# Kernel tuning notes

Hardware: AMD Instinct MI355X
Metric: run time of the kernel (lower is better)

The kernel has to match this reference:

```python
import jax, jax.numpy as jnp
import numpy as np

DIM = 1024
HEADS = 16
HEAD_DIM = DIM // HEADS
MLP_HIDDEN = DIM * 4
EPS = 1e-6


def _ln(x):
    # LayerNorm without affine, eps=1e-6
    mu = jnp.mean(x, axis=-1, keepdims=True)
    var = jnp.var(x, axis=-1, keepdims=True)
    return (x - mu) / jnp.sqrt(var + EPS)


def setup_inputs() -> dict:
    key = jax.random.key(0)
    ks = jax.random.split(key, 12)
    B, N = 8, 1024
    s = lambda fan: 1.0 / np.sqrt(fan)
    return {
        "x": jax.random.normal(ks[0], (B, N, DIM), jnp.float32),
        "c": jax.random.normal(ks[1], (B, DIM), jnp.float32),
        "w_qkv": jax.random.normal(ks[2], (DIM, 3 * DIM), jnp.float32) * s(DIM),
        "b_qkv": jnp.zeros((3 * DIM,), jnp.float32),
        "w_proj": jax.random.normal(ks[3], (DIM, DIM), jnp.float32) * s(DIM),
        "b_proj": jnp.zeros((DIM,), jnp.float32),
        "w_mlp1": jax.random.normal(ks[4], (DIM, MLP_HIDDEN), jnp.float32) * s(DIM),
        "b_mlp1": jnp.zeros((MLP_HIDDEN,), jnp.float32),
        "w_mlp2": jax.random.normal(ks[5], (MLP_HIDDEN, DIM), jnp.float32) * s(MLP_HIDDEN),
        "b_mlp2": jnp.zeros((DIM,), jnp.float32),
        "w_ada": jax.random.normal(ks[6], (DIM, 6 * DIM), jnp.float32) * s(DIM),
        "b_ada": jnp.zeros((6 * DIM,), jnp.float32),
    }


def _attention(h, w_qkv, b_qkv, w_proj, b_proj):
    B, N, C = h.shape
    qkv = h @ w_qkv + b_qkv  # [B,N,3C]
    qkv = qkv.reshape(B, N, 3, HEADS, HEAD_DIM)
    q, k, v = qkv[:, :, 0], qkv[:, :, 1], qkv[:, :, 2]  # [B,N,H,Dh]
    scale = HEAD_DIM ** -0.5
    attn = jnp.einsum("bqhd,bkhd->bhqk", q, k) * scale
    attn = jax.nn.softmax(attn, axis=-1)
    o = jnp.einsum("bhqk,bkhd->bqhd", attn, v).reshape(B, N, C)
    return o @ w_proj + b_proj


def reference(x, c, w_qkv, b_qkv, w_proj, b_proj, w_mlp1, b_mlp1, w_mlp2, b_mlp2, w_ada, b_ada):
    mod = (jax.nn.silu(c) @ w_ada + b_ada)[:, None, :]  # [B,1,6D]
    g1, be1, a1, g2, be2, a2 = jnp.split(mod, 6, axis=-1)
    h = _ln(x) * (1.0 + g1) + be1
    x = x + a1 * _attention(h, w_qkv, b_qkv, w_proj, b_proj)
    h = _ln(x) * (1.0 + g2) + be2
    mlp = jax.nn.gelu(h @ w_mlp1 + b_mlp1, approximate=False) @ w_mlp2 + b_mlp2
    return x + a2 * mlp
```

## Files before the change

kernel.cpp:

```cpp
#include <hip/hip_runtime.h>
#include <hip/hip_bf16.h>

#define DIMC 1024
#define SEQ  1024
#define NB   8
#define NH   16
#define HD2  64
#define EPSV 1e-6f

typedef short short8 __attribute__((ext_vector_type(8)));
typedef float floatx4 __attribute__((ext_vector_type(4)));

#define GLOAD_LDS(g, l) \
  __builtin_amdgcn_global_load_lds((const __attribute__((address_space(1))) unsigned int*)(g), \
                                   (__attribute__((address_space(3))) unsigned int*)(l), 16, 0, 0)

__device__ __forceinline__ float bf2f(unsigned short u){
  union { float f; unsigned int i; } v; v.i = ((unsigned int)u) << 16; return v.f;
}
__device__ __forceinline__ unsigned short f2bf(float f){
  union { float f; unsigned int i; } v; v.f = f;
  unsigned int r = v.i + 0x7fffu + ((v.i >> 16) & 1u);
  return (unsigned short)(r >> 16);
}

__global__ __launch_bounds__(256)
void tcvt_kernel(const float* __restrict__ in, unsigned short* __restrict__ out, int K, int N)
{
  __shared__ float tile[32][33];
  const int n0 = blockIdx.x * 32;
  const int k0 = blockIdx.y * 32;
  const int tx = threadIdx.x & 31;
  const int ty = threadIdx.x >> 5;
#pragma unroll
  for (int i = 0; i < 4; i++)
    tile[ty + i*8][tx] = in[(size_t)(k0 + ty + i*8) * N + n0 + tx];
  __syncthreads();
#pragma unroll
  for (int i = 0; i < 4; i++)
    out[(size_t)(n0 + ty + i*8) * K + k0 + tx] = f2bf(tile[tx][ty + i*8]);
}

__global__ __launch_bounds__(256)
void ada1_kernel(const float* __restrict__ c,
                 const float* __restrict__ w_ada,
                 float* __restrict__ partial)
{
  __shared__ float cs[NB][128];
  const int chunk = blockIdx.y;
  const int col = blockIdx.x * 256 + threadIdx.x;
  const int t = threadIdx.x;
  for (int i = t; i < NB * 128; i += 256) {
    const int b = i >> 7, k = i & 127;
    const float v = c[b * DIMC + chunk * 128 + k];
    cs[b][k] = v / (1.0f + __expf(-v));
  }
  __syncthreads();
  float acc[NB];
#pragma unroll
  for (int b = 0; b < NB; b++) acc[b] = 0.0f;
#pragma unroll 8
  for (int k = 0; k < 128; k++) {
    const float wv = w_ada[(size_t)(chunk * 128 + k) * 6144 + col];
#pragma unroll
    for (int b = 0; b < NB; b++) acc[b] = fmaf(cs[b][k], wv, acc[b]);
  }
#pragma unroll
  for (int b = 0; b < NB; b++)
    partial[((size_t)chunk * NB + b) * 6144 + col] = acc[b];
}

__global__ __launch_bounds__(256)
void ada2_kernel(const float* __restrict__ partial, const float* __restrict__ b_ada,
                 float* __restrict__ mod)
{
  const int i = blockIdx.x * 256 + threadIdx.x;
  const int b = i / 6144, col = i % 6144;
  float s = b_ada[col];
#pragma unroll
  for (int ch = 0; ch < 8; ch++) s += partial[((size_t)ch * NB + b) * 6144 + col];
  mod[i] = s;
}

__global__ __launch_bounds__(256)
void ln_kernel(const float* __restrict__ xin, const float* __restrict__ mod,
               int goff, int boff, unsigned short* __restrict__ hout)
{
  const int row = blockIdx.x;
  const int bb = row >> 10;
  const int t = threadIdx.x;
  const float4 x4 = *((const float4*)(xin + (size_t)row * DIMC) + t);
  const float v0 = x4.x, v1 = x4.y, v2 = x4.z, v3 = x4.w;
  float s  = v0 + v1 + v2 + v3;
  float ss = v0*v0 + v1*v1 + v2*v2 + v3*v3;
#pragma unroll
  for (int off = 32; off > 0; off >>= 1) {
    s  += __shfl_down(s,  off, 64);
    ss += __shfl_down(ss, off, 64);
  }
  __shared__ float red[10];
  const int w = t >> 6;
  if ((t & 63) == 0) { red[w] = s; red[4 + w] = ss; }
  __syncthreads();
  if (t == 0) {
    const float S  = red[0] + red[1] + red[2] + red[3];
    const float SS = red[4] + red[5] + red[6] + red[7];
    const float mu = S * (1.0f / 1024.0f);
    red[8] = mu;
    red[9] = rsqrtf(SS * (1.0f / 1024.0f) - mu * mu + EPSV);
  }
  __syncthreads();
  const float mu = red[8], rstd = red[9];
  const float* mrow = mod + (size_t)bb * 6144;
  const int d = t * 4;
  const float h0 = (v0 - mu) * rstd * (1.0f + mrow[goff + d + 0]) + mrow[boff + d + 0];
  const float h1 = (v1 - mu) * rstd * (1.0f + mrow[goff + d + 1]) + mrow[boff + d + 1];
  const float h2 = (v2 - mu) * rstd * (1.0f + mrow[goff + d + 2]) + mrow[boff + d + 2];
  const float h3 = (v3 - mu) * rstd * (1.0f + mrow[goff + d + 3]) + mrow[boff + d + 3];
  uint2 u;
  u.x = (unsigned)f2bf(h0) | ((unsigned)f2bf(h1) << 16);
  u.y = (unsigned)f2bf(h2) | ((unsigned)f2bf(h3) << 16);
  *((uint2*)(hout + (size_t)row * DIMC + d)) = u;
}

template<int MODE>
__global__ __launch_bounds__(256, 2)
void gemm_kernel(const unsigned short* __restrict__ A,
                 const unsigned short* __restrict__ Bt,
                 const float* __restrict__ bias,
                 void* __restrict__ Cout,
                 const float* __restrict__ resid,
                 const float* __restrict__ mod,
                 int M, int N, int K, int SH)
{
  __shared__ unsigned short As[128 * 32];
  __shared__ unsigned short Bs[128 * 32];
  const int tid = threadIdx.x;

  const int nT = N >> 7;
  const int mT = M >> 7;
  const int mb = mT >> 3;
  const int bid = blockIdx.x;
  const int xcd = bid & 7;
  const int slot = bid >> 3;
  const int sgroup = slot / (SH * nT);
  const int rem = slot - sgroup * (SH * nT);
  const int ni = rem / SH;
  const int mi = sgroup * SH + rem - ni * SH;
  const int m0 = (xcd * mb + mi) * 128;
  const int n0 = ni * 128;

  const int wid = tid >> 6;
  const int lane = tid & 63;
  const int quad = lane >> 4;
  const int c16 = lane & 15;
  const int wr = (wid >> 1) * 64;
  const int wc = (wid & 1) * 64;
  const int srow = lane >> 2;
  const int scol = (lane & 3) * 8;
  const unsigned short* aG = A  + (size_t)(m0 + wid * 32 + srow) * K + scol;
  const unsigned short* bG = Bt + (size_t)(n0 + wid * 32 + srow) * K + scol;
  unsigned short* AsW = As + wid * 32 * 32;
  unsigned short* BsW = Bs + wid * 32 * 32;

  floatx4 acc[4][4];
#pragma unroll
  for (int i = 0; i < 4; i++)
#pragma unroll
    for (int j = 0; j < 4; j++) acc[i][j] = (floatx4)(0.0f);

  for (int k0 = 0; k0 < K; k0 += 32) {
    GLOAD_LDS(aG + k0,            AsW);
    GLOAD_LDS(aG + 16 * K + k0,   AsW + 16 * 32);
    GLOAD_LDS(bG + k0,            BsW);
    GLOAD_LDS(bG + 16 * K + k0,   BsW + 16 * 32);
    __syncthreads();

    short8 af[4], bfv[4];
#pragma unroll
    for (int i = 0; i < 4; i++)
      af[i] = *(const short8*)&As[(wr + i * 16 + c16) * 32 + quad * 8];
#pragma unroll
    for (int j = 0; j < 4; j++)
      bfv[j] = *(const short8*)&Bs[(wc + j * 16 + c16) * 32 + quad * 8];
#pragma unroll
    for (int i = 0; i < 4; i++)
#pragma unroll
      for (int j = 0; j < 4; j++)
        acc[i][j] = __builtin_amdgcn_mfma_f32_16x16x32_bf16(af[i], bfv[j], acc[i][j], 0, 0, 0);
    __syncthreads();
  }

  const int bb = m0 >> 10;
#pragma unroll
  for (int j = 0; j < 4; j++) {
    const int col = n0 + wc + j * 16 + c16;
    const float bv = bias[col];
#pragma unroll
    for (int i = 0; i < 4; i++) {
      const int rowb = m0 + wr + i * 16 + quad * 4;
#pragma unroll
      for (int r = 0; r < 4; r++) {
        const int row = rowb + r;
        const size_t idx = (size_t)row * N + col;
        float v = acc[i][j][r] + bv;
        if (MODE == 0) {
          ((unsigned short*)Cout)[idx] = f2bf(v);
        } else if (MODE == 1) {
          v = 0.5f * v * (1.0f + erff(v * 0.70710678f));
          ((unsigned short*)Cout)[idx] = f2bf(v);
        } else if (MODE == 2) {
          const float a = mod[(size_t)bb * 6144 + 2048 + col];
          ((float*)Cout)[idx] = fmaf(a, v, resid[idx]);
        } else {
          const float a = mod[(size_t)bb * 6144 + 5120 + col];
          ((float*)Cout)[idx] = fmaf(a, v, resid[idx]);
        }
      }
    }
  }
}

__global__ __launch_bounds__(256, 2)
void fattn_kernel(const unsigned short* __restrict__ qkv, unsigned short* __restrict__ o_out)
{
  __shared__ unsigned short Ks[64][72];
  __shared__ unsigned short Vt[64][72];
  __shared__ unsigned short Pt[4][32][72];

  const int blk = blockIdx.x;
  const int qt = blk & 7;
  const int h  = (blk >> 3) & 15;
  const int bb = blk >> 7;
  const int tid = threadIdx.x;
  const int w = tid >> 6;
  const int lane = tid & 63;
  const int quad = lane >> 4;
  const int c16 = lane & 15;
  const int q0 = qt * 128 + w * 32;

  short8 qf[2][2];
#pragma unroll
  for (int msub = 0; msub < 2; msub++)
#pragma unroll
    for (int kh = 0; kh < 2; kh++) {
      const size_t idx = ((size_t)((bb*SEQ + q0 + msub*16 + c16) * 3 + 0)) * DIMC
                       + h * HD2 + kh * 32 + quad * 8;
      const uint4 u = *(const uint4*)(qkv + idx);
      const unsigned short* pu = (const unsigned short*)&u;
      short8 r;
#pragma unroll
      for (int j = 0; j < 8; j++) r[j] = (short)f2bf(bf2f(pu[j]) * 0.125f);
      qf[msub][kh] = r;
    }

  floatx4 oacc[2][4];
  float lsum[2][4];
#pragma unroll
  for (int msub = 0; msub < 2; msub++) {
#pragma unroll
    for (int r = 0; r < 4; r++) lsum[msub][r] = 0.0f;
#pragma unroll
    for (int d = 0; d < 4; d++) oacc[msub][d] = (floatx4)(0.0f);
  }

  const int tok = tid & 63;
  const int dg = tid >> 6;

  for (int kt = 0; kt < 16; kt++) {
    __syncthreads();
    {
      const size_t base = ((size_t)((bb*SEQ + kt*64 + tok) * 3)) * DIMC + h * HD2 + dg * 16;
      const uint4 ku0 = *(const uint4*)(qkv + base + DIMC);
      const uint4 ku1 = *(const uint4*)(qkv + base + DIMC + 8);
      const uint4 vu0 = *(const uint4*)(qkv + base + 2*DIMC);
      const uint4 vu1 = *(const uint4*)(qkv + base + 2*DIMC + 8);
      *(uint4*)&Ks[tok][dg*16]     = ku0;
      *(uint4*)&Ks[tok][dg*16 + 8] = ku1;
      const unsigned short* vp0 = (const unsigned short*)&vu0;
      const unsigned short* vp1 = (const unsigned short*)&vu1;
#pragma unroll
      for (int j = 0; j < 8; j++) Vt[dg*16 + j][tok] = vp0[j];
#pragma unroll
      for (int j = 0; j < 8; j++) Vt[dg*16 + 8 + j][tok] = vp1[j];
    }
    __syncthreads();

    floatx4 s[2][4];
#pragma unroll
    for (int msub = 0; msub < 2; msub++)
#pragma unroll
      for (int nsub = 0; nsub < 4; nsub++) s[msub][nsub] = (floatx4)(0.0f);
#pragma unroll
    for (int nsub = 0; nsub < 4; nsub++) {
      const short8 kf0 = *(const short8*)&Ks[nsub*16 + c16][quad*8];
      const short8 kf1 = *(const short8*)&Ks[nsub*16 + c16][32 + quad*8];
#pragma unroll
      for (int msub = 0; msub < 2; msub++) {
        s[msub][nsub] = __builtin_amdgcn_mfma_f32_16x16x32_bf16(qf[msub][0], kf0, s[msub][nsub], 0, 0, 0);
        s[msub][nsub] = __builtin_amdgcn_mfma_f32_16x16x32_bf16(qf[msub][1], kf1, s[msub][nsub], 0, 0, 0);
      }
    }

#pragma unroll
    for (int msub = 0; msub < 2; msub++)
#pragma unroll
      for (int nsub = 0; nsub < 4; nsub++)
#pragma unroll
        for (int r = 0; r < 4; r++) {
          const float p = __expf(s[msub][nsub][r] - 8.0f);
          lsum[msub][r] += p;
          Pt[w][msub*16 + quad*4 + r][nsub*16 + c16] = f2bf(p);
        }

    short8 pa[2][2];
#pragma unroll
    for (int msub = 0; msub < 2; msub++) {
      pa[msub][0] = *(const short8*)&Pt[w][msub*16 + c16][quad*8];
      pa[msub][1] = *(const short8*)&Pt[w][msub*16 + c16][32 + quad*8];
    }
#pragma unroll
    for (int dsub = 0; dsub < 4; dsub++) {
      const short8 vf0 = *(const short8*)&Vt[dsub*16 + c16][quad*8];
      const short8 vf1 = *(const short8*)&Vt[dsub*16 + c16][32 + quad*8];
#pragma unroll
      for (int msub = 0; msub < 2; msub++) {
        oacc[msub][dsub] = __builtin_amdgcn_mfma_f32_16x16x32_bf16(pa[msub][0], vf0, oacc[msub][dsub], 0, 0, 0);
        oacc[msub][dsub] = __builtin_amdgcn_mfma_f32_16x16x32_bf16(pa[msub][1], vf1, oacc[msub][dsub], 0, 0, 0);
      }
    }
  }

#pragma unroll
  for (int msub = 0; msub < 2; msub++) {
    float rl[4];
#pragma unroll
    for (int r = 0; r < 4; r++) {
      float t = lsum[msub][r];
#pragma unroll
      for (int xm = 1; xm < 16; xm <<= 1) t += __shfl_xor(t, xm, 64);
      rl[r] = 1.0f / t;
    }
#pragma unroll
    for (int dsub = 0; dsub < 4; dsub++)
#pragma unroll
      for (int r = 0; r < 4; r++) {
        const size_t idx = (size_t)(bb*SEQ + q0 + msub*16 + quad*4 + r) * DIMC
                         + h * HD2 + dsub*16 + c16;
        o_out[idx] = f2bf(oacc[msub][dsub][r] * rl[r]);
      }
  }
}

extern "C" void kernel_launch(void* const* d_in, const int* in_sizes, int n_in,
                              void* d_out, int out_size, void* d_ws, size_t ws_size,
                              hipStream_t stream) {
  const float* x      = (const float*)d_in[0];
  const float* c      = (const float*)d_in[1];
  const float* w_qkv  = (const float*)d_in[2];
  const float* b_qkv  = (const float*)d_in[3];
  const float* w_proj = (const float*)d_in[4];
  const float* b_proj = (const float*)d_in[5];
  const float* w_mlp1 = (const float*)d_in[6];
  const float* b_mlp1 = (const float*)d_in[7];
  const float* w_mlp2 = (const float*)d_in[8];
  const float* b_mlp2 = (const float*)d_in[9];
  const float* w_ada  = (const float*)d_in[10];
  const float* b_ada  = (const float*)d_in[11];

  char* ws = (char*)d_ws;
  float*          mod     = (float*)(ws);
  unsigned short* wqkv_t  = (unsigned short*)(ws + 196608);
  unsigned short* wproj_t = (unsigned short*)(ws + 6488064);
  unsigned short* wmlp1_t = (unsigned short*)(ws + 8585216);
  unsigned short* wmlp2_t = (unsigned short*)(ws + 16973824);
  unsigned short* bufH    = (unsigned short*)(ws + 25362432);
  float*          adapart = (float*)(ws + 25362432);
  unsigned short* qkv     = (unsigned short*)(ws + 42139648);
  unsigned short* hid     = (unsigned short*)(ws + 42139648);
  float*          out     = (float*)d_out;

  const int M = NB * SEQ;

  tcvt_kernel<<<dim3(96, 32),  256, 0, stream>>>(w_qkv,  wqkv_t,  1024, 3072);
  tcvt_kernel<<<dim3(32, 32),  256, 0, stream>>>(w_proj, wproj_t, 1024, 1024);
  tcvt_kernel<<<dim3(128, 32), 256, 0, stream>>>(w_mlp1, wmlp1_t, 1024, 4096);
  tcvt_kernel<<<dim3(32, 128), 256, 0, stream>>>(w_mlp2, wmlp2_t, 4096, 1024);

  ada1_kernel<<<dim3(24, 8), 256, 0, stream>>>(c, w_ada, adapart);
  ada2_kernel<<<192, 256, 0, stream>>>(adapart, b_ada, mod);

  ln_kernel<<<M, 256, 0, stream>>>(x, mod, 0, 1024, bufH);
  gemm_kernel<0><<<24 * 64, 256, 0, stream>>>(bufH, wqkv_t, b_qkv, qkv, nullptr, nullptr, M, 3072, 1024, 8);
  fattn_kernel<<<1024, 256, 0, stream>>>(qkv, bufH);
  gemm_kernel<2><<<8 * 64, 256, 0, stream>>>(bufH, wproj_t, b_proj, out, x, mod, M, 1024, 1024, 8);
  ln_kernel<<<M, 256, 0, stream>>>(out, mod, 3072, 4096, bufH);

  const size_t fullHidEnd = 42139648ull + (size_t)M * 4096 * 2;
  if (ws_size >= fullHidEnd) {
    gemm_kernel<1><<<32 * 64, 256, 0, stream>>>(bufH, wmlp1_t, b_mlp1, hid,
                                                nullptr, nullptr, M, 4096, 1024, 8);
    gemm_kernel<3><<<8 * 64, 256, 0, stream>>>(hid, wmlp2_t, b_mlp2, out,
                                               out, mod, M, 1024, 4096, 2);
  } else {
    for (int half = 0; half < 2; half++) {
      const size_t roff = (size_t)half * 4096;
      gemm_kernel<1><<<32 * 32, 256, 0, stream>>>(bufH + roff * DIMC, wmlp1_t, b_mlp1, hid,
                                                  nullptr, nullptr, 4096, 4096, 1024, 4);
      gemm_kernel<3><<<8 * 32, 256, 0, stream>>>(hid, wmlp2_t, b_mlp2, out + roff * DIMC,
                                                 out + roff * DIMC, mod + (size_t)half * 4 * 6144,
                                                 4096, 1024, 4096, 2);
    }
  }
}
```

Before: 556.0 us.

## Replace 128x128 GEMM with double-buffered 256x256 tile, 8-wave pipelined kernel

Rewrites the GEMM as a 256x256 output tile with 512 threads and a K-step of 64. LDS is double-buffered and XOR-swizzled, and the global->LDS loads for the next k-slice are interleaved with MFMA phases under explicit barriers, vmcnt waits and setprio. Larger tiles raise operand reuse per byte loaded, and the software pipelining hides load latency behind MFMA work. In exchange it uses 128KB of LDS per block and heavy register pressure. Grid sizes shrink, for example only 128 blocks for the N=1024 GEMMs, which may leave CUs idle.

```diff
diff --git a/kernel.cpp b/kernel.cpp
--- a/kernel.cpp
+++ b/kernel.cpp
@@ -123,82 +123,134 @@
   *((uint2*)(hout + (size_t)row * DIMC + d)) = u;
 }
 
+#define MF(a, b, c) __builtin_amdgcn_mfma_f32_16x16x32_bf16(a, b, c, 0, 0, 0)
+#define FENCE() asm volatile("" ::: "memory")
+#define BARRIER() do { FENCE(); __builtin_amdgcn_s_barrier(); FENCE(); } while (0)
+
 template<int MODE>
-__global__ __launch_bounds__(256, 2)
-void gemm_kernel(const unsigned short* __restrict__ A,
-                 const unsigned short* __restrict__ Bt,
-                 const float* __restrict__ bias,
-                 void* __restrict__ Cout,
-                 const float* __restrict__ resid,
-                 const float* __restrict__ mod,
-                 int M, int N, int K, int SH)
-{
-  __shared__ unsigned short As[128 * 32];
-  __shared__ unsigned short Bs[128 * 32];
-  const int tid = threadIdx.x;
-
-  const int nT = N >> 7;
-  const int mT = M >> 7;
+__global__ __launch_bounds__(512, 2)
+void gemm256_kernel(const unsigned short* __restrict__ A,
+                    const unsigned short* __restrict__ Bt,
+                    const float* __restrict__ bias,
+                    void* __restrict__ Cout,
+                    const float* __restrict__ resid,
+                    const float* __restrict__ mod,
+                    int M, int N, int K)
+{
+  __shared__ unsigned short As[2][16384];
+  __shared__ unsigned short Bs[2][16384];
+
+  const int mT = M >> 8;
   const int mb = mT >> 3;
   const int bid = blockIdx.x;
   const int xcd = bid & 7;
-  const int slot = bid >> 3;
-  const int sgroup = slot / (SH * nT);
-  const int rem = slot - sgroup * (SH * nT);
-  const int ni = rem / SH;
-  const int mi = sgroup * SH + rem - ni * SH;
-  const int m0 = (xcd * mb + mi) * 128;
-  const int n0 = ni * 128;
-
-  const int wid = tid >> 6;
-  const int lane = tid & 63;
-  const int quad = lane >> 4;
-  const int c16 = lane & 15;
-  const int wr = (wid >> 1) * 64;
-  const int wc = (wid & 1) * 64;
-  const int srow = lane >> 2;
-  const int scol = (lane & 3) * 8;
-  const unsigned short* aG = A  + (size_t)(m0 + wid * 32 + srow) * K + scol;
-  const unsigned short* bG = Bt + (size_t)(n0 + wid * 32 + srow) * K + scol;
-  unsigned short* AsW = As + wid * 32 * 32;
-  unsigned short* BsW = Bs + wid * 32 * 32;
-
-  floatx4 acc[4][4];
-#pragma unroll
-  for (int i = 0; i < 4; i++)
+  const int local = bid >> 3;
+  const int ni = local / mb;
+  const int mi = xcd * mb + (local - ni * mb);
+  const int m0 = mi << 8, n0 = ni << 8;
+
+  const int tid = threadIdx.x;
+  const int w = tid >> 6, lane = tid & 63;
+  const int quad = lane >> 4, c16 = lane & 15;
+  const int wm = w >> 2, wn = w & 3, w2 = w << 1;
+
+  const int aRow = wm * 8192 + c16 * 64;
+  const int bRow = (wn >> 1) * 8192 + ((wn & 1) * 64 + c16) * 64;
+  const int sxz  = (c16 & 7) << 4;
+  const int swz0 = ((0  + quad * 16) ^ sxz) >> 1;
+  const int swz1 = ((64 + quad * 16) ^ sxz) >> 1;
+#define LDA8(cc, i, SW) (*(const short8*)&As[cc][aRow + (i) * 1024 + (SW)])
+#define LDB8(cc, j, SW) (*(const short8*)&Bs[cc][bRow + (j) * 1024 + (SW)])
+
+  const int l8 = lane >> 3, lc = lane & 7;
+  const int stC = ((lc ^ l8) << 3);
+  const unsigned short* aSt = A  + (size_t)(m0 + w2 * 8 + l8) * K + stC;
+  const unsigned short* bSt = Bt + (size_t)(n0 + w2 * 8 + l8) * K + stC;
+#define STAGE_A(cc, h, kk0) do { \
+  GLOAD_LDS(aSt + (size_t)((h) * 128    ) * K + (kk0), &As[cc][(h) * 8192 + w2 * 512      ]); \
+  GLOAD_LDS(aSt + (size_t)((h) * 128 + 8) * K + (kk0), &As[cc][(h) * 8192 + w2 * 512 + 512]); \
+} while (0)
+#define STAGE_B(cc, h, kk0) do { \
+  GLOAD_LDS(bSt + (size_t)((h) * 128    ) * K + (kk0), &Bs[cc][(h) * 8192 + w2 * 512      ]); \
+  GLOAD_LDS(bSt + (size_t)((h) * 128 + 8) * K + (kk0), &Bs[cc][(h) * 8192 + w2 * 512 + 512]); \
+} while (0)
+
+  floatx4 acc[8][4];
+#pragma unroll
+  for (int i = 0; i < 8; i++)
 #pragma unroll
     for (int j = 0; j < 4; j++) acc[i][j] = (floatx4)(0.0f);
 
-  for (int k0 = 0; k0 < K; k0 += 32) {
-    GLOAD_LDS(aG + k0,            AsW);
-    GLOAD_LDS(aG + 16 * K + k0,   AsW + 16 * 32);
-    GLOAD_LDS(bG + k0,            BsW);
-    GLOAD_LDS(bG + 16 * K + k0,   BsW + 16 * 32);
-    __syncthreads();
-
-    short8 af[4], bfv[4];
-#pragma unroll
-    for (int i = 0; i < 4; i++)
-      af[i] = *(const short8*)&As[(wr + i * 16 + c16) * 32 + quad * 8];
-#pragma unroll
-    for (int j = 0; j < 4; j++)
-      bfv[j] = *(const short8*)&Bs[(wc + j * 16 + c16) * 32 + quad * 8];
-#pragma unroll
-    for (int i = 0; i < 4; i++)
-#pragma unroll
-      for (int j = 0; j < 4; j++)
-        acc[i][j] = __builtin_amdgcn_mfma_f32_16x16x32_bf16(af[i], bfv[j], acc[i][j], 0, 0, 0);
-    __syncthreads();
+#define MMROW(i, aE, aO) do { \
+  acc[i][0] = MF(aE, bF00, acc[i][0]); acc[i][0] = MF(aO, bF01, acc[i][0]); \
+  acc[i][1] = MF(aE, bF10, acc[i][1]); acc[i][1] = MF(aO, bF11, acc[i][1]); \
+  acc[i][2] = MF(aE, bF20, acc[i][2]); acc[i][2] = MF(aO, bF21, acc[i][2]); \
+  acc[i][3] = MF(aE, bF30, acc[i][3]); acc[i][3] = MF(aO, bF31, acc[i][3]); \
+} while (0)
+
+#define PH_TAIL(i0, i1) do { \
+  BARRIER(); \
+  asm volatile("s_waitcnt lgkmcnt(0)" ::: "memory"); \
+  __builtin_amdgcn_s_setprio(1); \
+  MMROW(i0, a0, a1); \
+  MMROW(i1, a2, a3); \
+  __builtin_amdgcn_s_setprio(0); \
+} while (0)
+
+#define GROUP(cc, oo, g) do { \
+  const int kA_ = ((g) + 1) << 6; const int kB_ = ((g) + 2) << 6; \
+  const bool dA_ = kA_ < K; const bool dB_ = kB_ < K; \
+  short8 bF00 = LDB8(cc, 0, swz0), bF01 = LDB8(cc, 0, swz1); \
+  short8 bF10 = LDB8(cc, 1, swz0), bF11 = LDB8(cc, 1, swz1); \
+  short8 bF20 = LDB8(cc, 2, swz0), bF21 = LDB8(cc, 2, swz1); \
+  short8 bF30 = LDB8(cc, 3, swz0), bF31 = LDB8(cc, 3, swz1); \
+  short8 a0 = LDA8(cc, 0, swz0), a1 = LDA8(cc, 0, swz1); \
+  short8 a2 = LDA8(cc, 1, swz0), a3 = LDA8(cc, 1, swz1); \
+  if (dA_) STAGE_A(oo, 0, kA_); \
+  PH_TAIL(0, 1); \
+  BARRIER(); \
+  a0 = LDA8(cc, 2, swz0); a1 = LDA8(cc, 2, swz1); \
+  a2 = LDA8(cc, 3, swz0); a3 = LDA8(cc, 3, swz1); \
+  if (dA_) STAGE_A(oo, 1, kA_); \
+  PH_TAIL(2, 3); \
+  BARRIER(); \
+  a0 = LDA8(cc, 4, swz0); a1 = LDA8(cc, 4, swz1); \
+  a2 = LDA8(cc, 5, swz0); a3 = LDA8(cc, 5, swz1); \
+  if (dB_) STAGE_B(cc, 0, kB_); \
+  PH_TAIL(4, 5); \
+  BARRIER(); \
+  a0 = LDA8(cc, 6, swz0); a1 = LDA8(cc, 6, swz1); \
+  a2 = LDA8(cc, 7, swz0); a3 = LDA8(cc, 7, swz1); \
+  if (dB_) STAGE_B(cc, 1, kB_); \
+  PH_TAIL(6, 7); \
+  if (dB_) { asm volatile("s_waitcnt vmcnt(4)" ::: "memory"); } \
+  else     { asm volatile("s_waitcnt vmcnt(0)" ::: "memory"); } \
+  BARRIER(); \
+} while (0)
+
+  STAGE_B(0, 0, 0);  STAGE_B(0, 1, 0);
+  STAGE_A(0, 0, 0);  STAGE_A(0, 1, 0);
+  STAGE_B(1, 0, 64); STAGE_B(1, 1, 64);
+  asm volatile("s_waitcnt vmcnt(4)" ::: "memory");
+  BARRIER();
+
+  const int T = K >> 6;
+  for (int g = 0; g < T; g += 2) {
+    GROUP(0, 1, g);
+    GROUP(1, 0, g + 1);
   }
 
   const int bb = m0 >> 10;
 #pragma unroll
   for (int j = 0; j < 4; j++) {
-    const int col = n0 + wc + j * 16 + c16;
+    const int col = n0 + wn * 64 + j * 16 + c16;
     const float bv = bias[col];
-#pragma unroll
-    for (int i = 0; i < 4; i++) {
-      const int rowb = m0 + wr + i * 16 + quad * 4;
+    float av = 0.0f;
+    if (MODE == 2) av = mod[(size_t)bb * 6144 + 2048 + col];
+    if (MODE == 3) av = mod[(size_t)bb * 6144 + 5120 + col];
+#pragma unroll
+    for (int i = 0; i < 8; i++) {
+      const int rowb = m0 + wm * 128 + i * 16 + quad * 4;
 #pragma unroll
       for (int r = 0; r < 4; r++) {
         const int row = rowb + r;
@@ -209,16 +261,19 @@
         } else if (MODE == 1) {
           v = 0.5f * v * (1.0f + erff(v * 0.70710678f));
           ((unsigned short*)Cout)[idx] = f2bf(v);
-        } else if (MODE == 2) {
-          const float a = mod[(size_t)bb * 6144 + 2048 + col];
-          ((float*)Cout)[idx] = fmaf(a, v, resid[idx]);
         } else {
-          const float a = mod[(size_t)bb * 6144 + 5120 + col];
-          ((float*)Cout)[idx] = fmaf(a, v, resid[idx]);
+          ((float*)Cout)[idx] = fmaf(av, v, resid[idx]);
         }
       }
     }
   }
+#undef GROUP
+#undef PH_TAIL
+#undef MMROW
+#undef STAGE_A
+#undef STAGE_B
+#undef LDA8
+#undef LDB8
 }
 
 __global__ __launch_bounds__(256, 2)
@@ -391,25 +446,25 @@
   ada2_kernel<<<192, 256, 0, stream>>>(adapart, b_ada, mod);
 
   ln_kernel<<<M, 256, 0, stream>>>(x, mod, 0, 1024, bufH);
-  gemm_kernel<0><<<24 * 64, 256, 0, stream>>>(bufH, wqkv_t, b_qkv, qkv, nullptr, nullptr, M, 3072, 1024, 8);
+  gemm256_kernel<0><<<384, 512, 0, stream>>>(bufH, wqkv_t, b_qkv, qkv, nullptr, nullptr, M, 3072, 1024);
   fattn_kernel<<<1024, 256, 0, stream>>>(qkv, bufH);
-  gemm_kernel<2><<<8 * 64, 256, 0, stream>>>(bufH, wproj_t, b_proj, out, x, mod, M, 1024, 1024, 8);
+  gemm256_kernel<2><<<128, 512, 0, stream>>>(bufH, wproj_t, b_proj, out, x, mod, M, 1024, 1024);
   ln_kernel<<<M, 256, 0, stream>>>(out, mod, 3072, 4096, bufH);
 
   const size_t fullHidEnd = 42139648ull + (size_t)M * 4096 * 2;
   if (ws_size >= fullHidEnd) {
-    gemm_kernel<1><<<32 * 64, 256, 0, stream>>>(bufH, wmlp1_t, b_mlp1, hid,
-                                                nullptr, nullptr, M, 4096, 1024, 8);
-    gemm_kernel<3><<<8 * 64, 256, 0, stream>>>(hid, wmlp2_t, b_mlp2, out,
-                                               out, mod, M, 1024, 4096, 2);
+    gemm256_kernel<1><<<512, 512, 0, stream>>>(bufH, wmlp1_t, b_mlp1, hid,
+                                               nullptr, nullptr, M, 4096, 1024);
+    gemm256_kernel<3><<<128, 512, 0, stream>>>(hid, wmlp2_t, b_mlp2, out,
+                                               out, mod, M, 1024, 4096);
   } else {
     for (int half = 0; half < 2; half++) {
       const size_t roff = (size_t)half * 4096;
-      gemm_kernel<1><<<32 * 32, 256, 0, stream>>>(bufH + roff * DIMC, wmlp1_t, b_mlp1, hid,
-                                                  nullptr, nullptr, 4096, 4096, 1024, 4);
-      gemm_kernel<3><<<8 * 32, 256, 0, stream>>>(hid, wmlp2_t, b_mlp2, out + roff * DIMC,
-                                                 out + roff * DIMC, mod + (size_t)half * 4 * 6144,
-                                                 4096, 1024, 4096, 2);
-    }
-  }
-}
+      gemm256_kernel<1><<<256, 512, 0, stream>>>(bufH + roff * DIMC, wmlp1_t, b_mlp1, hid,
+                                                 nullptr, nullptr, 4096, 4096, 1024);
+      gemm256_kernel<3><<<64, 512, 0, stream>>>(hid, wmlp2_t, b_mlp2, out + roff * DIMC,
+                                                out + roff * DIMC, mod + (size_t)half * 4 * 6144,
+                                                4096, 1024, 4096);
+    }
+  }
+}
```

After: 586.1 us. 1.05x slower.
